# Performance work log

Measured on AMD Instinct MI355X. Metric: run time of the kernel, lower is better.

The kernel has to match this reference:

```python
import jax, jax.numpy as jnp
import numpy as np

B, S, D_MODEL, H = 2, 2048, 1024, 16
DEPTH = D_MODEL // H


def setup_inputs() -> dict:
    key = jax.random.key(0)
    ks = jax.random.split(key, 12)
    s = 1.0 / np.sqrt(D_MODEL)
    inp = {
        "q": jax.random.normal(ks[0], (B, S, D_MODEL), jnp.float32),
        "k": jax.random.normal(ks[1], (B, S, D_MODEL), jnp.float32),
        "v": jax.random.normal(ks[2], (B, S, D_MODEL), jnp.float32),
        # CTRL-style causal mask: 1 where position is disallowed (future), 0 otherwise
        "mask": jnp.triu(jnp.ones((S, S), jnp.float32), k=1),
        "Wq_w": jax.random.normal(ks[3], (D_MODEL, D_MODEL), jnp.float32) * s,
        "Wq_b": jax.random.normal(ks[4], (D_MODEL,), jnp.float32) * s,
        "Wk_w": jax.random.normal(ks[5], (D_MODEL, D_MODEL), jnp.float32) * s,
        "Wk_b": jax.random.normal(ks[6], (D_MODEL,), jnp.float32) * s,
        "Wv_w": jax.random.normal(ks[7], (D_MODEL, D_MODEL), jnp.float32) * s,
        "Wv_b": jax.random.normal(ks[8], (D_MODEL,), jnp.float32) * s,
        "dense_w": jax.random.normal(ks[9], (D_MODEL, D_MODEL), jnp.float32) * s,
        "dense_b": jax.random.normal(ks[10], (D_MODEL,), jnp.float32) * s,
    }
    return inp


def _split_heads(x):
    # [B, S, D] -> [B, H, S, depth]
    b, s, _ = x.shape
    return x.reshape(b, s, H, DEPTH).transpose(0, 2, 1, 3)


def reference(q, k, v, mask, Wq_w, Wq_b, Wk_w, Wk_b, Wv_w, Wv_b, dense_w, dense_b):
    b = q.shape[0]
    # torch Linear: y = x @ W^T + b
    qh = _split_heads(q @ Wq_w.T + Wq_b)  # [B,H,Sq,dh]
    kh = _split_heads(k @ Wk_w.T + Wk_b)  # [B,H,Sk,dh]
    vh = _split_heads(v @ Wv_w.T + Wv_b)  # [B,H,Sk,dh]

    scale = 1.0 / np.sqrt(DEPTH)
    logits = jnp.einsum("bhqd,bhkd->bhqk", qh, kh) * scale  # [B,H,Sq,Sk]
    nd, ns = logits.shape[-2], logits.shape[-1]
    logits = logits + mask[ns - nd:ns, :ns] * -10000.0
    attn = jax.nn.softmax(logits, axis=-1)
    ctx = jnp.einsum("bhqk,bhkd->bhqd", attn, vh)  # [B,H,Sq,dh]
    ctx = ctx.transpose(0, 2, 1, 3).reshape(b, -1, D_MODEL)  # [B,Sq,D]
    out = ctx @ dense_w.T + dense_b
    return out
```

## Files before the change

### kernel.cpp

```cpp
#include <hip/hip_runtime.h>
#include <hip/hip_bf16.h>

typedef __bf16 bf16x8 __attribute__((ext_vector_type(8)));
typedef __bf16 bf16x4 __attribute__((ext_vector_type(4)));
typedef float  f32x4  __attribute__((ext_vector_type(4)));

#define D_MODEL 1024
#define SEQ     2048
#define NH      16
#define DH      64
#define MTOT    4096

__device__ __forceinline__ void gload16(const void* gp, void* lp) {
  __builtin_amdgcn_global_load_lds(
      (const __attribute__((address_space(1))) unsigned int*)gp,
      (__attribute__((address_space(3))) unsigned int*)lp,
      16, 0, 0);
}

struct CvtSegs {
  const float* s[7];
  __bf16*      d[7];
  int          n8[7];
};

__global__ __launch_bounds__(256) void cvt_kernel(CvtSegs c) {
  const int seg = blockIdx.y;
  const float4* s = (const float4*)c.s[seg];
  bf16x8*       d = (bf16x8*)c.d[seg];
  const int n8 = c.n8[seg];
  for (int i = blockIdx.x * 256 + threadIdx.x; i < n8; i += gridDim.x * 256) {
    float4 a = s[2 * i];
    float4 b = s[2 * i + 1];
    bf16x8 o;
    o[0] = (__bf16)a.x; o[1] = (__bf16)a.y; o[2] = (__bf16)a.z; o[3] = (__bf16)a.w;
    o[4] = (__bf16)b.x; o[5] = (__bf16)b.y; o[6] = (__bf16)b.z; o[7] = (__bf16)b.w;
    d[i] = o;
  }
}

template <int EPI>
__device__ __forceinline__ void gemm_core(const __bf16* __restrict__ A,
                                          const __bf16* __restrict__ W,
                                          const float* __restrict__ bias,
                                          void* __restrict__ outp,
                                          __bf16* Asm, __bf16* Bsm,
                                          int row0, int col0) {
  const int tid = threadIdx.x;
  const int lane = tid & 63;
  const int w = tid >> 6;
  const int lr = lane & 15, lg = lane >> 4;
  const int wr = w >> 1, wc = w & 1;
  char* AsB = (char*)Asm;
  char* BsB = (char*)Bsm;

  f32x4 acc[4][4];
#pragma unroll
  for (int i = 0; i < 4; ++i)
#pragma unroll
    for (int j = 0; j < 4; ++j) acc[i][j] = (f32x4){0.f, 0.f, 0.f, 0.f};

  const int kch = (lane & 3) * 8;

#pragma unroll
  for (int s = 0; s < 2; ++s) {
    const int cb = (w * 2 + s) * 64;
    const int arow = (cb + lane) >> 2;
    gload16(A + (size_t)(row0 + arow) * D_MODEL + kch, AsB + cb * 16);
    gload16(W + (size_t)(col0 + arow) * D_MODEL + kch, BsB + cb * 16);
  }

  int cur = 0;
  for (int t = 0; t < 32; ++t) {
    __syncthreads();
    if (t + 1 < 32) {
      const int nxt = cur ^ 1;
      const int k0 = (t + 1) * 32;
#pragma unroll
      for (int s = 0; s < 2; ++s) {
        const int cb = (w * 2 + s) * 64;
        const int arow = (cb + lane) >> 2;
        gload16(A + (size_t)(row0 + arow) * D_MODEL + k0 + kch,
                AsB + nxt * 8192 + cb * 16);
        gload16(W + (size_t)(col0 + arow) * D_MODEL + k0 + kch,
                BsB + nxt * 8192 + cb * 16);
      }
    }
    {
      char* Ab = AsB + cur * 8192;
      char* Bb = BsB + cur * 8192;
      bf16x8 af[4], bfr[4];
#pragma unroll
      for (int mi = 0; mi < 4; ++mi)
        af[mi] = *(const bf16x8*)(Ab + (wr * 64 + mi * 16 + lr) * 64 + lg * 16);
#pragma unroll
      for (int ni = 0; ni < 4; ++ni)
        bfr[ni] = *(const bf16x8*)(Bb + (wc * 64 + ni * 16 + lr) * 64 + lg * 16);
      __builtin_amdgcn_s_setprio(1);
#pragma unroll
      for (int mi = 0; mi < 4; ++mi)
#pragma unroll
        for (int ni = 0; ni < 4; ++ni)
          acc[mi][ni] = __builtin_amdgcn_mfma_f32_16x16x32_bf16(af[mi], bfr[ni],
                                                                acc[mi][ni], 0, 0, 0);
      __builtin_amdgcn_s_setprio(0);
    }
    cur ^= 1;
  }

  if (EPI == 2) {
    __bf16* o = (__bf16*)outp;
#pragma unroll
    for (int mi = 0; mi < 4; ++mi) {
#pragma unroll
      for (int ni = 0; ni < 4; ++ni) {
        const int n = col0 + wc * 64 + ni * 16 + lr;
        const float bv = bias[n];
        const int m0 = row0 + wr * 64 + mi * 16 + lg * 4;
        bf16x4 pk;
#pragma unroll
        for (int j = 0; j < 4; ++j) pk[j] = (__bf16)(acc[mi][ni][j] + bv);
        *(bf16x4*)(o + ((size_t)((m0 >> 11) * NH + (n >> 6)) * DH + (n & 63)) * SEQ +
                   (m0 & 2047)) = pk;
      }
    }
  } else {
#pragma unroll
    for (int mi = 0; mi < 4; ++mi) {
#pragma unroll
      for (int ni = 0; ni < 4; ++ni) {
        const int n = col0 + wc * 64 + ni * 16 + lr;
        const float bv = bias[n];
#pragma unroll
        for (int j = 0; j < 4; ++j) {
          const int m = row0 + wr * 64 + mi * 16 + lg * 4 + j;
          const float v = acc[mi][ni][j] + bv;
          if (EPI == 0) {
            __bf16* o = (__bf16*)outp;
            o[(size_t)((m >> 11) * NH + (n >> 6)) * (SEQ * DH) +
              (size_t)(m & 2047) * DH + (n & 63)] = (__bf16)v;
          } else {
            float* o = (float*)outp;
            o[(size_t)m * D_MODEL + n] = v;
          }
        }
      }
    }
  }
}

struct QkvPtrs {
  const __bf16* A[3];
  const __bf16* W[3];
  const float*  b[3];
  __bf16*       o[3];
};

__global__ __launch_bounds__(256) void gemm_qkv_kernel(QkvPtrs p) {
  __shared__ __bf16 As[2][128 * 32];
  __shared__ __bf16 Bs[2][128 * 32];
  const int z = blockIdx.z;
  if (z == 2)
    gemm_core<2>(p.A[z], p.W[z], p.b[z], p.o[z], &As[0][0], &Bs[0][0],
                 blockIdx.x * 128, blockIdx.y * 128);
  else
    gemm_core<0>(p.A[z], p.W[z], p.b[z], p.o[z], &As[0][0], &Bs[0][0],
                 blockIdx.x * 128, blockIdx.y * 128);
}

__global__ __launch_bounds__(256) void gemm_out_kernel(const __bf16* __restrict__ A,
                                                       const __bf16* __restrict__ W,
                                                       const float* __restrict__ b,
                                                       float* __restrict__ o) {
  __shared__ __bf16 As[2][128 * 32];
  __shared__ __bf16 Bs[2][128 * 32];
  gemm_core<1>(A, W, b, o, &As[0][0], &Bs[0][0], blockIdx.x * 128, blockIdx.y * 128);
}

__global__ __launch_bounds__(256, 4) void attn_kernel(const __bf16* __restrict__ qh,
                                                      const __bf16* __restrict__ kh,
                                                      const __bf16* __restrict__ vt,
                                                      __bf16* __restrict__ ctx) {
  __shared__ __bf16 Ks[2][64 * 64];
  __shared__ __bf16 Vt[2][64 * 64];
  __shared__ __bf16 Ps[4][16 * 64];

  const int bh = blockIdx.x;
  const int qb = 31 - blockIdx.y;
  const int tid = threadIdx.x, lane = tid & 63, w = tid >> 6;
  const int lr = lane & 15, lg = lane >> 4;
  const size_t hoff = (size_t)bh * SEQ * DH;
  const __bf16* Q   = qh + hoff;
  const __bf16* Kp  = kh + hoff;
  const __bf16* Vtp = vt + hoff;
  const int q0 = qb * 64 + w * 16;

  bf16x8 qf[2];
#pragma unroll
  for (int ki = 0; ki < 2; ++ki)
    qf[ki] = *(const bf16x8*)(Q + (size_t)(q0 + lr) * DH + ki * 32 + lg * 8);

  f32x4 o[4];
#pragma unroll
  for (int ni = 0; ni < 4; ++ni) o[ni] = (f32x4){0.f, 0.f, 0.f, 0.f};
  float lsum = 0.f;

  char* Psw = (char*)Ps[w];
  const int nt = qb + 1;

#pragma unroll
  for (int s = 0; s < 2; ++s) {
    const int c = (w * 2 + s) * 64 + lane;
    const int row = c >> 3;
    const int gch = (c & 7) ^ (row & 7);
    gload16(Kp + (size_t)row * DH + gch * 8, (char*)Ks[0] + (w * 2 + s) * 1024);
    gload16(Vtp + (size_t)row * SEQ + gch * 8, (char*)Vt[0] + (w * 2 + s) * 1024);
  }

  int cur = 0;
  for (int t = 0; t < nt; ++t) {
    __syncthreads();
    if (t + 1 < nt) {
      const int nxt = cur ^ 1;
#pragma unroll
      for (int s = 0; s < 2; ++s) {
        const int c = (w * 2 + s) * 64 + lane;
        const int row = c >> 3;
        const int gch = (c & 7) ^ (row & 7);
        gload16(Kp + (size_t)((t + 1) * 64 + row) * DH + gch * 8,
                (char*)Ks[nxt] + (w * 2 + s) * 1024);
        gload16(Vtp + (size_t)row * SEQ + (t + 1) * 64 + gch * 8,
                (char*)Vt[nxt] + (w * 2 + s) * 1024);
      }
    }
    {
      char* KsB = (char*)Ks[cur];
      char* VtB = (char*)Vt[cur];

      f32x4 st[4];
#pragma unroll
      for (int ni = 0; ni < 4; ++ni) st[ni] = (f32x4){0.f, 0.f, 0.f, 0.f};
      __builtin_amdgcn_s_setprio(1);
#pragma unroll
      for (int ki = 0; ki < 2; ++ki) {
        const int kc = ki * 4 + lg;
#pragma unroll
        for (int ni = 0; ni < 4; ++ni) {
          const int row = ni * 16 + lr;
          bf16x8 kf = *(const bf16x8*)(KsB + row * 128 + ((kc ^ (row & 7)) << 4));
          st[ni] = __builtin_amdgcn_mfma_f32_16x16x32_bf16(kf, qf[ki], st[ni], 0, 0, 0);
        }
      }
      __builtin_amdgcn_s_setprio(0);

      const int kvb = t * 64;
      const bool needmask = (kvb + 63 > q0);
      const int q = q0 + lr;
      float p[4][4];
      float psum = 0.f;
#pragma unroll
      for (int ni = 0; ni < 4; ++ni) {
#pragma unroll
        for (int j = 0; j < 4; ++j) {
          float v = st[ni][j] * 0.18033688f;
          if (needmask && (kvb + ni * 16 + lg * 4 + j > q)) v = -1e9f;
          const float pe = __builtin_amdgcn_exp2f(v);
          p[ni][j] = pe;
          psum += pe;
        }
      }
      lsum += psum;

#pragma unroll
      for (int ni = 0; ni < 4; ++ni) {
        bf16x4 pk;
#pragma unroll
        for (int j = 0; j < 4; ++j) pk[j] = (__bf16)p[ni][j];
        const int chunk = 2 * ni + (lg >> 1);
        *(bf16x4*)(Psw + lr * 128 + ((chunk ^ (lr & 7)) << 4) + (lg & 1) * 8) = pk;
      }
      asm volatile("s_waitcnt lgkmcnt(0)" ::: "memory");
      __builtin_amdgcn_sched_barrier(0);

      __builtin_amdgcn_s_setprio(1);
#pragma unroll
      for (int ki = 0; ki < 2; ++ki) {
        const int kc = ki * 4 + lg;
        bf16x8 pf2 = *(const bf16x8*)(Psw + lr * 128 + ((kc ^ (lr & 7)) << 4));
#pragma unroll
        for (int ni = 0; ni < 4; ++ni) {
          const int d = ni * 16 + lr;
          bf16x8 vf = *(const bf16x8*)(VtB + d * 128 + ((kc ^ (lr & 7)) << 4));
          o[ni] = __builtin_amdgcn_mfma_f32_16x16x32_bf16(pf2, vf, o[ni], 0, 0, 0);
        }
      }
      __builtin_amdgcn_s_setprio(0);
    }
    cur ^= 1;
  }

  lsum += __shfl_xor(lsum, 16, 64);
  lsum += __shfl_xor(lsum, 32, 64);
  const int bb = bh >> 4, hh = bh & 15;
#pragma unroll
  for (int j = 0; j < 4; ++j) {
    const int row = lg * 4 + j;
    const float inv = 1.0f / __shfl(lsum, row, 64);
    const int qrow = q0 + row;
    __bf16* orow = ctx + (size_t)(bb * SEQ + qrow) * D_MODEL + hh * DH;
#pragma unroll
    for (int ni = 0; ni < 4; ++ni)
      orow[ni * 16 + lr] = (__bf16)(o[ni][j] * inv);
  }
}

extern "C" void kernel_launch(void* const* d_in, const int* in_sizes, int n_in,
                              void* d_out, int out_size, void* d_ws, size_t ws_size,
                              hipStream_t stream) {
  (void)in_sizes; (void)n_in; (void)out_size; (void)ws_size;
  const float* q  = (const float*)d_in[0];
  const float* k  = (const float*)d_in[1];
  const float* v  = (const float*)d_in[2];
  const float* Wq = (const float*)d_in[4];
  const float* bq = (const float*)d_in[5];
  const float* Wk = (const float*)d_in[6];
  const float* bk = (const float*)d_in[7];
  const float* Wv = (const float*)d_in[8];
  const float* bv = (const float*)d_in[9];
  const float* Wd = (const float*)d_in[10];
  const float* bd = (const float*)d_in[11];

  char* ws = (char*)d_ws;
  __bf16* qb  = (__bf16*)(ws + 0);
  __bf16* kb  = (__bf16*)(ws + 8388608);
  __bf16* vb  = (__bf16*)(ws + 16777216);
  __bf16* wqb = (__bf16*)(ws + 25165824);
  __bf16* wkb = (__bf16*)(ws + 27262976);
  __bf16* wvb = (__bf16*)(ws + 29360128);
  __bf16* wdb = (__bf16*)(ws + 31457280);
  __bf16* qhp = (__bf16*)(ws + 33554432);
  __bf16* khp = (__bf16*)(ws + 41943040);
  __bf16* vtp = (__bf16*)(ws + 50331648);
  __bf16* ctxp= (__bf16*)(ws + 58720256);

  CvtSegs cs;
  cs.s[0] = q;  cs.d[0] = qb;  cs.n8[0] = 524288;
  cs.s[1] = k;  cs.d[1] = kb;  cs.n8[1] = 524288;
  cs.s[2] = v;  cs.d[2] = vb;  cs.n8[2] = 524288;
  cs.s[3] = Wq; cs.d[3] = wqb; cs.n8[3] = 131072;
  cs.s[4] = Wk; cs.d[4] = wkb; cs.n8[4] = 131072;
  cs.s[5] = Wv; cs.d[5] = wvb; cs.n8[5] = 131072;
  cs.s[6] = Wd; cs.d[6] = wdb; cs.n8[6] = 131072;
  cvt_kernel<<<dim3(256, 7, 1), dim3(256), 0, stream>>>(cs);

  QkvPtrs qp;
  qp.A[0] = qb;  qp.A[1] = kb;  qp.A[2] = vb;
  qp.W[0] = wqb; qp.W[1] = wkb; qp.W[2] = wvb;
  qp.b[0] = bq;  qp.b[1] = bk;  qp.b[2] = bv;
  qp.o[0] = qhp; qp.o[1] = khp; qp.o[2] = vtp;
  gemm_qkv_kernel<<<dim3(32, 8, 3), dim3(256), 0, stream>>>(qp);

  attn_kernel<<<dim3(32, 32, 1), dim3(256), 0, stream>>>(qhp, khp, vtp, ctxp);

  gemm_out_kernel<<<dim3(32, 8, 1), dim3(256), 0, stream>>>(ctxp, wdb, bd, (float*)d_out);
}
```

Before: 120.0 us.

## Triple-buffer GEMM LDS tiles with explicit vmcnt waits and single barrier

Turns the shared GEMM core's double-buffered global-to-LDS pipeline into a three-stage ring. Loads run two K-steps ahead, and each iteration waits with an explicit s_waitcnt vmcnt instead of a full __syncthreads. This gives global loads more time to land under the MFMA work of earlier tiles. In exchange, LDS per block grows to 48KB and launch bounds now request 3 blocks per CU, which may limit occupancy or register allocation. The modulo-3 buffer indexing and the hand-written waitcnt counts must match the number of loads in flight.

```diff
diff --git a/kernel.cpp b/kernel.cpp
--- a/kernel.cpp
+++ b/kernel.cpp
@@ -63,32 +63,38 @@
   const int kch = (lane & 3) * 8;
 
 #pragma unroll
-  for (int s = 0; s < 2; ++s) {
-    const int cb = (w * 2 + s) * 64;
-    const int arow = (cb + lane) >> 2;
-    gload16(A + (size_t)(row0 + arow) * D_MODEL + kch, AsB + cb * 16);
-    gload16(W + (size_t)(col0 + arow) * D_MODEL + kch, BsB + cb * 16);
-  }
-
-  int cur = 0;
+  for (int tt = 0; tt < 2; ++tt) {
+#pragma unroll
+    for (int s = 0; s < 2; ++s) {
+      const int cb = (w * 2 + s) * 64;
+      const int arow = (cb + lane) >> 2;
+      gload16(A + (size_t)(row0 + arow) * D_MODEL + tt * 32 + kch,
+              AsB + tt * 8192 + cb * 16);
+      gload16(W + (size_t)(col0 + arow) * D_MODEL + tt * 32 + kch,
+              BsB + tt * 8192 + cb * 16);
+    }
+  }
+
   for (int t = 0; t < 32; ++t) {
-    __syncthreads();
-    if (t + 1 < 32) {
-      const int nxt = cur ^ 1;
-      const int k0 = (t + 1) * 32;
+    if (t < 31) asm volatile("s_waitcnt vmcnt(4)" ::: "memory");
+    else        asm volatile("s_waitcnt vmcnt(0)" ::: "memory");
+    __builtin_amdgcn_s_barrier();
+    if (t + 2 < 32) {
+      const int nb = (t + 2) % 3;
+      const int k0 = (t + 2) * 32;
 #pragma unroll
       for (int s = 0; s < 2; ++s) {
         const int cb = (w * 2 + s) * 64;
         const int arow = (cb + lane) >> 2;
         gload16(A + (size_t)(row0 + arow) * D_MODEL + k0 + kch,
-                AsB + nxt * 8192 + cb * 16);
+                AsB + nb * 8192 + cb * 16);
         gload16(W + (size_t)(col0 + arow) * D_MODEL + k0 + kch,
-                BsB + nxt * 8192 + cb * 16);
+                BsB + nb * 8192 + cb * 16);
       }
     }
     {
-      char* Ab = AsB + cur * 8192;
-      char* Bb = BsB + cur * 8192;
+      char* Ab = AsB + (t % 3) * 8192;
+      char* Bb = BsB + (t % 3) * 8192;
       bf16x8 af[4], bfr[4];
 #pragma unroll
       for (int mi = 0; mi < 4; ++mi)
@@ -104,8 +110,8 @@
           acc[mi][ni] = __builtin_amdgcn_mfma_f32_16x16x32_bf16(af[mi], bfr[ni],
                                                                 acc[mi][ni], 0, 0, 0);
       __builtin_amdgcn_s_setprio(0);
-    }
-    cur ^= 1;
+      __builtin_amdgcn_sched_barrier(0);
+    }
   }
 
   if (EPI == 2) {
@@ -156,9 +162,9 @@
   __bf16*       o[3];
 };
 
-__global__ __launch_bounds__(256) void gemm_qkv_kernel(QkvPtrs p) {
-  __shared__ __bf16 As[2][128 * 32];
-  __shared__ __bf16 Bs[2][128 * 32];
+__global__ __launch_bounds__(256, 3) void gemm_qkv_kernel(QkvPtrs p) {
+  __shared__ __bf16 As[3][128 * 32];
+  __shared__ __bf16 Bs[3][128 * 32];
   const int z = blockIdx.z;
   if (z == 2)
     gemm_core<2>(p.A[z], p.W[z], p.b[z], p.o[z], &As[0][0], &Bs[0][0],
@@ -168,12 +174,12 @@
                  blockIdx.x * 128, blockIdx.y * 128);
 }
 
-__global__ __launch_bounds__(256) void gemm_out_kernel(const __bf16* __restrict__ A,
-                                                       const __bf16* __restrict__ W,
-                                                       const float* __restrict__ b,
-                                                       float* __restrict__ o) {
-  __shared__ __bf16 As[2][128 * 32];
-  __shared__ __bf16 Bs[2][128 * 32];
+__global__ __launch_bounds__(256, 3) void gemm_out_kernel(const __bf16* __restrict__ A,
+                                                          const __bf16* __restrict__ W,
+                                                          const float* __restrict__ b,
+                                                          float* __restrict__ o) {
+  __shared__ __bf16 As[3][128 * 32];
+  __shared__ __bf16 Bs[3][128 * 32];
   gemm_core<1>(A, W, b, o, &As[0][0], &Bs[0][0], blockIdx.x * 128, blockIdx.y * 128);
 }
 
```

After: 117.1 us. 2.4% less time.
